# Kernel tuning notes

Measured on AMD Instinct MI355X. Metric: run time of the kernel, lower is better.

Reference implementation:

```python
import jax, jax.numpy as jnp
import numpy as np

N = 100000   # nodes
E = 1600000  # edges (avg degree 16)
IN, H, OUT = 64, 128, 1


def setup_inputs() -> dict:
    key = jax.random.key(0)
    ks = jax.random.split(key, 12)
    s = 0.05
    return {
        "x": jax.random.normal(ks[0], (N, IN), jnp.float32),
        "edge_index": jax.random.randint(ks[1], (2, E), 0, N, dtype=jnp.int64),
        "Wl1": jax.random.normal(ks[2], (IN, H), jnp.float32) * s,
        "Wr1": jax.random.normal(ks[3], (IN, H), jnp.float32) * s,
        "b1": jnp.zeros((H,), jnp.float32),
        "ln_g": jnp.ones((H,), jnp.float32),
        "ln_b": jnp.zeros((H,), jnp.float32),
        "Wres": jax.random.normal(ks[4], (IN, H), jnp.float32) * s,
        "bres": jnp.zeros((H,), jnp.float32),
        "Wl2": jax.random.normal(ks[5], (H, H), jnp.float32) * s,
        "Wr2": jax.random.normal(ks[6], (H, H), jnp.float32) * s,
        "b2": jnp.zeros((H,), jnp.float32),
        "Wl3": jax.random.normal(ks[7], (H, H), jnp.float32) * s,
        "Wr3": jax.random.normal(ks[8], (H, H), jnp.float32) * s,
        "b3": jnp.zeros((H,), jnp.float32),
        "Wl4": jax.random.normal(ks[9], (H, OUT), jnp.float32) * s,
        "Wr4": jax.random.normal(ks[10], (H, OUT), jnp.float32) * s,
        "b4": jnp.zeros((OUT,), jnp.float32),
    }


def _sage(h, src, dst, deg_inv, Wl, Wr, b):
    # PyG SAGEConv, aggr='mean': lin_l(mean_{j in N(i)} h_j) + lin_r(h_i)
    agg = jax.ops.segment_sum(h[src], dst, num_segments=N) * deg_inv[:, None]
    return agg @ Wl + h @ Wr + b


def _layernorm(h, g, b, eps=1e-5):
    mu = jnp.mean(h, axis=-1, keepdims=True)
    var = jnp.mean((h - mu) ** 2, axis=-1, keepdims=True)
    return (h - mu) * jax.lax.rsqrt(var + eps) * g + b


def reference(x, edge_index, Wl1, Wr1, b1, ln_g, ln_b, Wres, bres,
              Wl2, Wr2, b2, Wl3, Wr3, b3, Wl4, Wr4, b4):
    src, dst = edge_index[0], edge_index[1]
    deg = jax.ops.segment_sum(jnp.ones((E,), jnp.float32), dst, num_segments=N)
    deg_inv = 1.0 / jnp.maximum(deg, 1.0)

    h = jax.nn.relu(_layernorm(_sage(x, src, dst, deg_inv, Wl1, Wr1, b1), ln_g, ln_b))
    h = h + x @ Wres + bres              # residual (in_channel != hidden_channel)
    h = jax.nn.relu(_sage(h, src, dst, deg_inv, Wl2, Wr2, b2))   # dropout: eval no-op
    h = jax.nn.relu(_sage(h, src, dst, deg_inv, Wl3, Wr3, b3))
    out = _sage(h, src, dst, deg_inv, Wl4, Wr4, b4)
    return out.squeeze(-1)
```

## Files before the change

### kernel.cpp

```cpp
#include <hip/hip_runtime.h>
#include <hip/hip_bf16.h>

#define N_NODES 100000
#define N_EDGES 1600000

#define NBKT 782
#define SCAT_BLOCKS 240
#define BKT_CHUNK 6667
#define LP 72

#define SORT_BLOCKS 40
#define SORT_CHUNK 2500
#define BH2_N (NBKT * SCAT_BLOCKS)
#define BHB ((BH2_N + 1023) / 1024)
#define XBF_BLOCKS 6250

typedef __attribute__((ext_vector_type(8))) short short8v;
typedef __attribute__((ext_vector_type(4))) float float4v;

__device__ __forceinline__ unsigned short f2bf(float f) {
    unsigned int u = __float_as_uint(f);
    u = (u + 0x7FFFu + ((u >> 16) & 1u)) >> 16;
    return (unsigned short)u;
}
__device__ __forceinline__ float bf2f(unsigned short b) {
    return __uint_as_float((unsigned int)b << 16);
}

__global__ __launch_bounds__(256) void hist_xbf_kernel(const int* __restrict__ ei, int* __restrict__ bh2,
                                                       const float* __restrict__ x, unsigned short* __restrict__ xcat) {
    __shared__ int h[NBKT];
    int tid = threadIdx.x;
    if (blockIdx.x < SCAT_BLOCKS) {
        for (int i = tid; i < NBKT; i += 256) h[i] = 0;
        __syncthreads();
        int start = blockIdx.x * BKT_CHUNK;
        int end = start + BKT_CHUNK; if (end > N_EDGES) end = N_EDGES;
        for (int i = start + tid; i < end; i += 256) {
            int d = ei[N_EDGES + i];
            atomicAdd(&h[d >> 7], 1);
        }
        __syncthreads();
        for (int i = tid; i < NBKT; i += 256) bh2[i * SCAT_BLOCKS + blockIdx.x] = h[i];
    } else {
        int idx = (blockIdx.x - SCAT_BLOCKS) * 256 + tid;
        if (idx < N_NODES * 16) {
            int node = idx >> 4;
            int f0 = (idx & 15) * 4;
            float4 v = *(const float4*)(x + (size_t)idx * 4);
            ushort4 o;
            o.x = f2bf(v.x); o.y = f2bf(v.y); o.z = f2bf(v.z); o.w = f2bf(v.w);
            *(ushort4*)(xcat + (size_t)node * 128 + f0) = o;
        }
    }
}

__global__ __launch_bounds__(256) void gscan_a_kernel(const int* __restrict__ in, int* __restrict__ bsum, int n) {
    __shared__ int lds[256];
    int tid = threadIdx.x;
    int base = blockIdx.x * 1024 + tid * 4;
    int s = 0;
    #pragma unroll
    for (int i = 0; i < 4; i++) s += (base + i < n) ? in[base + i] : 0;
    lds[tid] = s;
    __syncthreads();
    for (int off = 128; off; off >>= 1) {
        if (tid < off) lds[tid] += lds[tid + off];
        __syncthreads();
    }
    if (tid == 0) bsum[blockIdx.x] = lds[0];
}

__global__ __launch_bounds__(256) void gscan_c_kernel(int* __restrict__ data, const int* __restrict__ bsum,
                                                      int nb, int n) {
    __shared__ int sb[256];
    __shared__ int lds[256];
    int tid = threadIdx.x;
    sb[tid] = (tid < nb) ? bsum[tid] : 0;
    __syncthreads();
    for (int off = 1; off < 256; off <<= 1) {
        int y = 0;
        if (tid >= off) y = sb[tid - off];
        __syncthreads();
        if (tid >= off) sb[tid] += y;
        __syncthreads();
    }
    int blockbase = (blockIdx.x == 0) ? 0 : sb[blockIdx.x - 1];

    int base = blockIdx.x * 1024 + tid * 4;
    int v[4];
    int s = 0;
    #pragma unroll
    for (int i = 0; i < 4; i++) {
        v[i] = (base + i < n) ? data[base + i] : 0;
        s += v[i];
    }
    lds[tid] = s;
    __syncthreads();
    for (int off = 1; off < 256; off <<= 1) {
        int y = 0;
        if (tid >= off) y = lds[tid - off];
        __syncthreads();
        if (tid >= off) lds[tid] += y;
        __syncthreads();
    }
    int run = blockbase + lds[tid] - s;
    #pragma unroll
    for (int i = 0; i < 4; i++) {
        if (base + i < n) data[base + i] = run;
        run += v[i];
// ... 157 lines not shown
}

__global__ __launch_bounds__(256) void agg128_kernel(unsigned short* __restrict__ hcat,
                                                     const int* __restrict__ row_ptr, const int* __restrict__ col,
                                                     const int* __restrict__ ord) {
    int tid = threadIdx.x;
    int slot = blockIdx.x * 8 + (tid >> 5);
    if (slot >= N_NODES) return;
    int i = ord[slot];
    int f0 = (tid & 31) * 4;
    int s = row_ptr[i], e = row_ptr[i + 1];
    float a0 = 0.f, a1 = 0.f, a2 = 0.f, a3 = 0.f;
    int t = s;
    while (t + 7 < e) {
        int j0 = col[t], j1 = col[t + 1], j2 = col[t + 2], j3 = col[t + 3];
        int j4 = col[t + 4], j5 = col[t + 5], j6 = col[t + 6], j7 = col[t + 7];
        ushort4 u0 = *(const ushort4*)(hcat + (size_t)j0 * 256 + f0);
        ushort4 u1 = *(const ushort4*)(hcat + (size_t)j1 * 256 + f0);
        ushort4 u2 = *(const ushort4*)(hcat + (size_t)j2 * 256 + f0);
        ushort4 u3 = *(const ushort4*)(hcat + (size_t)j3 * 256 + f0);
        ushort4 u4 = *(const ushort4*)(hcat + (size_t)j4 * 256 + f0);
        ushort4 u5 = *(const ushort4*)(hcat + (size_t)j5 * 256 + f0);
        ushort4 u6 = *(const ushort4*)(hcat + (size_t)j6 * 256 + f0);
        ushort4 u7 = *(const ushort4*)(hcat + (size_t)j7 * 256 + f0);
        ACC4(u0) ACC4(u1) ACC4(u2) ACC4(u3) ACC4(u4) ACC4(u5) ACC4(u6) ACC4(u7)
        t += 8;
    }
    if (t + 3 < e) {
        int j0 = col[t], j1 = col[t + 1], j2 = col[t + 2], j3 = col[t + 3];
        ushort4 u0 = *(const ushort4*)(hcat + (size_t)j0 * 256 + f0);
        ushort4 u1 = *(const ushort4*)(hcat + (size_t)j1 * 256 + f0);
        ushort4 u2 = *(const ushort4*)(hcat + (size_t)j2 * 256 + f0);
        ushort4 u3 = *(const ushort4*)(hcat + (size_t)j3 * 256 + f0);
        ACC4(u0) ACC4(u1) ACC4(u2) ACC4(u3)
        t += 4;
    }
    if (t + 1 < e) {
        int j0 = col[t], j1 = col[t + 1];
        ushort4 u0 = *(const ushort4*)(hcat + (size_t)j0 * 256 + f0);
        ushort4 u1 = *(const ushort4*)(hcat + (size_t)j1 * 256 + f0);
        ACC4(u0) ACC4(u1)
        t += 2;
    }
    if (t < e) {
        ushort4 u0 = *(const ushort4*)(hcat + (size_t)col[t] * 256 + f0);
        ACC4(u0)
    }
    float di = 1.0f / fmaxf((float)(e - s), 1.0f);
    ushort4 o;
    o.x = f2bf(a0 * di); o.y = f2bf(a1 * di); o.z = f2bf(a2 * di); o.w = f2bf(a3 * di);
    *(ushort4*)(hcat + (size_t)i * 256 + 128 + f0) = o;
}

__global__ __launch_bounds__(256) void wprep_all_kernel(const float* __restrict__ Wr1, const float* __restrict__ Wl1,
                                                        const float* __restrict__ Wres,
                                                        const float* __restrict__ Wl2, const float* __restrict__ Wr2,
                                                        const float* __restrict__ Wl3, const float* __restrict__ Wr3,
                                                        unsigned short* __restrict__ Bt1,
                                                        unsigned short* __restrict__ Bt2,
                                                        unsigned short* __restrict__ Bt3) {
    int idx = blockIdx.x * 256 + threadIdx.x;
    int seg = idx >> 15;
    int loc = idx & 32767;
    if (seg == 0) {
        int n = loc >> 7;
        int k = loc & 127;
        float v;
        if (n < 128) v = (k < 64) ? Wr1[k * 128 + n] : Wl1[(k - 64) * 128 + n];
        else         v = (k < 64) ? Wres[k * 128 + (n - 128)] : 0.f;
        Bt1[loc] = f2bf(v);
    } else if (seg == 1) {
        int n = loc >> 8;
        int k = loc & 255;
        float v = (k < 128) ? Wr2[k * 128 + n] : Wl2[(k - 128) * 128 + n];
        Bt2[loc] = f2bf(v);
    } else if (seg == 2) {
        int n = loc >> 8;
        int k = loc & 255;
        float v = (k < 128) ? Wr3[k * 128 + n] : Wl3[(k - 128) * 128 + n];
        Bt3[loc] = f2bf(v);
    }
}

__global__ __launch_bounds__(256) void mgemm1_ln_kernel(const unsigned short* __restrict__ A,
                                                        const unsigned short* __restrict__ Bt, int M,
                                                        const float* __restrict__ b1, const float* __restrict__ ln_g,
                                                        const float* __restrict__ ln_b, const float* __restrict__ bres,
                                                        unsigned short* __restrict__ hcat) {
    __shared__ unsigned short As[128 * LP];
    __shared__ unsigned short Bs[256 * LP];
    __shared__ float lsum[2][128], lsq[2][128];
    int tid = threadIdx.x;
    int m0 = blockIdx.x * 128;

    int lane = tid & 63;
    int wave = tid >> 6;
    int wm = (wave & 1) * 64;
    int wn = (wave >> 1) * 64;
    int lm = lane & 15;
    int lk = (lane >> 4) * 8;

    float4v accT[4][4], accR[4][4];
    #pragma unroll
    for (int i = 0; i < 4; i++)
        #pragma unroll
        for (int j = 0; j < 4; j++) { accT[i][j] = (float4v)0.f; accR[i][j] = (float4v)0.f; }

    int sr = tid >> 3;
    int sc = (tid & 7) * 8;

    for (int ks = 0; ks < 128; ks += 64) {
        if (ks) __syncthreads();
        int kk = ks + sc;
        #pragma unroll
        for (int rr = 0; rr < 384; rr += 32) {
            int r = sr + rr;
            if (r < 128) {
                int gm = m0 + r; if (gm > M - 1) gm = M - 1;
                *(ulonglong2*)&As[r * LP + sc] = *(const ulonglong2*)(A + (size_t)gm * 128 + kk);
            } else {
                int br = r - 128;
                *(ulonglong2*)&Bs[br * LP + sc] = *(const ulonglong2*)(Bt + (size_t)br * 128 + kk);
            }
        }
        __syncthreads();

        #pragma unroll
        for (int k0 = 0; k0 < 64; k0 += 32) {
            short8v af[4], bfT[4], bfR[4];
            #pragma unroll
            for (int i = 0; i < 4; i++)
                af[i] = *(const short8v*)&As[(wm + i * 16 + lm) * LP + k0 + lk];
            #pragma unroll
            for (int j = 0; j < 4; j++) {
                bfT[j] = *(const short8v*)&Bs[(wn + j * 16 + lm) * LP + k0 + lk];
                bfR[j] = *(const short8v*)&Bs[(128 + wn + j * 16 + lm) * LP + k0 + lk];
            }
            #pragma unroll
            for (int i = 0; i < 4; i++)
                #pragma unroll
                for (int j = 0; j < 4; j++) {
                    accT[i][j] = __builtin_amdgcn_mfma_f32_16x16x32_bf16(af[i], bfT[j], accT[i][j], 0, 0, 0);
                    accR[i][j] = __builtin_amdgcn_mfma_f32_16x16x32_bf16(af[i], bfR[j], accR[i][j], 0, 0, 0);
                }
        }
    }

    int q = lane >> 4;
    int wnidx = wave >> 1;
    float b1v[4], gv[4], bbv[4], brv[4];
    #pragma unroll
    for (int j = 0; j < 4; j++) {
        int cc = wn + j * 16 + lm;
        b1v[j] = b1[cc]; gv[j] = ln_g[cc]; bbv[j] = ln_b[cc]; brv[j] = bres[cc];
    }
    #pragma unroll
    for (int i = 0; i < 4; i++) {
        #pragma unroll
        for (int r = 0; r < 4; r++) {
            float sp = 0.f, sq = 0.f;
            #pragma unroll
            for (int j = 0; j < 4; j++) {
                float tv = accT[i][j][r] + b1v[j];
                sp += tv; sq += tv * tv;
            }
            #pragma unroll
            for (int off = 1; off < 16; off <<= 1) {
                sp += __shfl_xor(sp, off);
                sq += __shfl_xor(sq, off);
            }
            if (lm == 0) {
                int m = wm + i * 16 + q * 4 + r;
                lsum[wnidx][m] = sp;
                lsq[wnidx][m] = sq;
            }
        }
    }
    __syncthreads();
    #pragma unroll
    for (int i = 0; i < 4; i++) {
        #pragma unroll
        for (int r = 0; r < 4; r++) {
            int m = wm + i * 16 + q * 4 + r;
            float sum = lsum[0][m] + lsum[1][m];
            float s2 = lsq[0][m] + lsq[1][m];
            float mu = sum * (1.f / 128.f);
            float var = s2 * (1.f / 128.f) - mu * mu;
            float rstd = rsqrtf(var + 1e-5f);
            int gm = m0 + m;
            if (gm < M) {
                #pragma unroll
                for (int j = 0; j < 4; j++) {
                    float tv = accT[i][j][r] + b1v[j];
                    float y = fmaxf((tv - mu) * rstd * gv[j] + bbv[j], 0.f) + accR[i][j][r] + brv[j];
                    hcat[(size_t)gm * 256 + wn + j * 16 + lm] = f2bf(y);
                }
            }
        }
    }
}

__global__ __launch_bounds__(256) void mgemm_kernel(const unsigned short* __restrict__ A, int lda,
                                                    const unsigned short* __restrict__ Bt, int M,
                                                    const float* __restrict__ bias,
                                                    unsigned short* __restrict__ C, int ldc) {
    __shared__ unsigned short As[128 * LP];
    __shared__ unsigned short Bs[128 * LP];
    int tid = threadIdx.x;
    int m0 = blockIdx.x * 128;
    int n0 = blockIdx.y * 128;

    int lane = tid & 63;
    int wave = tid >> 6;
    int wm = (wave & 1) * 64;
    int wn = (wave >> 1) * 64;
    int lm = lane & 15;
    int lk = (lane >> 4) * 8;

    float4v acc[4][4];
    #pragma unroll
    for (int i = 0; i < 4; i++)
        #pragma unroll
        for (int j = 0; j < 4; j++) acc[i][j] = (float4v)0.f;

    int sr = tid >> 3;
    int sc = (tid & 7) * 8;

    for (int ks = 0; ks < lda; ks += 64) {
        if (ks) __syncthreads();
        int kk = ks + sc;
        #pragma unroll
        for (int rr = 0; rr < 128; rr += 32) {
            int r = sr + rr;
            int gm = m0 + r; if (gm > M - 1) gm = M - 1;
            *(ulonglong2*)&As[r * LP + sc] = *(const ulonglong2*)(A + (size_t)gm * lda + kk);
            *(ulonglong2*)&Bs[r * LP + sc] = *(const ulonglong2*)(Bt + (size_t)(n0 + r) * lda + kk);
        }
        __syncthreads();

        #pragma unroll
        for (int k0 = 0; k0 < 64; k0 += 32) {
            short8v af[4], bf[4];
            #pragma unroll
            for (int i = 0; i < 4; i++)
                af[i] = *(const short8v*)&As[(wm + i * 16 + lm) * LP + k0 + lk];
            #pragma unroll
            for (int j = 0; j < 4; j++)
                bf[j] = *(const short8v*)&Bs[(wn + j * 16 + lm) * LP + k0 + lk];
            #pragma unroll
            for (int i = 0; i < 4; i++)
                #pragma unroll
                for (int j = 0; j < 4; j++)
                    acc[i][j] = __builtin_amdgcn_mfma_f32_16x16x32_bf16(af[i], bf[j], acc[i][j], 0, 0, 0);
        }
    }

    int r0b = (lane >> 4) * 4;
    #pragma unroll
    for (int i = 0; i < 4; i++) {
        #pragma unroll
        for (int j = 0; j < 4; j++) {
            int cc = n0 + wn + j * 16 + lm;
            float bv = (bias != nullptr) ? bias[cc] : 0.f;
            #pragma unroll
            for (int r = 0; r < 4; r++) {
                int m = m0 + wm + i * 16 + r0b + r;
                if (m < M) {
                    float v = acc[i][j][r];
                    if (bias != nullptr) v = fmaxf(v + bv, 0.f);
                    C[(size_t)m * ldc + cc] = f2bf(v);
                }
            }
        }
    }
}

__global__ __launch_bounds__(256) void mgemm_pq_kernel(const unsigned short* __restrict__ A, int lda,
                                                       const unsigned short* __restrict__ Bt, int M,
                                                       const float* __restrict__ bias,
                                                       const float* __restrict__ Wl4, const float* __restrict__ Wr4,
                                                       const float* __restrict__ b4,
                                                       float* __restrict__ p, float* __restrict__ q) {
    __shared__ unsigned short As[128 * LP];
    __shared__ unsigned short Bs[128 * LP];
    __shared__ float psA[2][128], qsA[2][128];
    int tid = threadIdx.x;
    int m0 = blockIdx.x * 128;

    int lane = tid & 63;
    int wave = tid >> 6;
    int wm = (wave & 1) * 64;
    int wn = (wave >> 1) * 64;
    int lm = lane & 15;
    int lk = (lane >> 4) * 8;

    float4v acc[4][4];
    #pragma unroll
    for (int i = 0; i < 4; i++)
        #pragma unroll
        for (int j = 0; j < 4; j++) acc[i][j] = (float4v)0.f;

    int sr = tid >> 3;
    int sc = (tid & 7) * 8;

    for (int ks = 0; ks < lda; ks += 64) {
        if (ks) __syncthreads();
        int kk = ks + sc;
        #pragma unroll
        for (int rr = 0; rr < 128; rr += 32) {
            int r = sr + rr;
            int gm = m0 + r; if (gm > M - 1) gm = M - 1;
            *(ulonglong2*)&As[r * LP + sc] = *(const ulonglong2*)(A + (size_t)gm * lda + kk);
            *(ulonglong2*)&Bs[r * LP + sc] = *(const ulonglong2*)(Bt + (size_t)r * lda + kk);
        }
        __syncthreads();

        #pragma unroll
        for (int k0 = 0; k0 < 64; k0 += 32) {
            short8v af[4], bf[4];
            #pragma unroll
            for (int i = 0; i < 4; i++)
                af[i] = *(const short8v*)&As[(wm + i * 16 + lm) * LP + k0 + lk];
            #pragma unroll
            for (int j = 0; j < 4; j++)
                bf[j] = *(const short8v*)&Bs[(wn + j * 16 + lm) * LP + k0 + lk];
            #pragma unroll
            for (int i = 0; i < 4; i++)
                #pragma unroll
                for (int j = 0; j < 4; j++)
                    acc[i][j] = __builtin_amdgcn_mfma_f32_16x16x32_bf16(af[i], bf[j], acc[i][j], 0, 0, 0);
        }
    }

    int qd = lane >> 4;
    int wnidx = wave >> 1;
    float b3v[4], wlv[4], wrv[4];
    #pragma unroll
    for (int j = 0; j < 4; j++) {
        int cc = wn + j * 16 + lm;
        b3v[j] = bias[cc]; wlv[j] = Wl4[cc]; wrv[j] = Wr4[cc];
    }
    #pragma unroll
    for (int i = 0; i < 4; i++) {
        #pragma unroll
        for (int r = 0; r < 4; r++) {
            float pp = 0.f, qq = 0.f;
            #pragma unroll
            for (int j = 0; j < 4; j++) {
                float hv = fmaxf(acc[i][j][r] + b3v[j], 0.f);
                pp += hv * wlv[j]; qq += hv * wrv[j];
            }
            #pragma unroll
            for (int off = 1; off < 16; off <<= 1) {
                pp += __shfl_xor(pp, off);
                qq += __shfl_xor(qq, off);
            }
            if (lm == 0) {
                int m = wm + i * 16 + qd * 4 + r;
                psA[wnidx][m] = pp;
                qsA[wnidx][m] = qq;
            }
        }
    }
    __syncthreads();
    if (wnidx == 0 && lm == 0) {
        float b4v = b4[0];
        #pragma unroll
        for (int i = 0; i < 4; i++) {
            #pragma unroll
            for (int r = 0; r < 4; r++) {
                int m = wm + i * 16 + qd * 4 + r;
                int gm = m0 + m;
                if (gm < M) {
                    p[gm] = psA[0][m] + psA[1][m];
                    q[gm] = qsA[0][m] + qsA[1][m] + b4v;
                }
            }
        }
    }
}

__global__ __launch_bounds__(256) void final_kernel(const float* __restrict__ p, const float* __restrict__ q,
                                                    const int* __restrict__ row_ptr, const int* __restrict__ col,
                                                    float* __restrict__ out) {
    int i = blockIdx.x * 256 + threadIdx.x;
    if (i >= N_NODES) return;
    int s = row_ptr[i], e = row_ptr[i + 1];
    float acc = 0.f;
    int t = s;
    for (; t + 3 < e; t += 4)
        acc += p[col[t]] + p[col[t + 1]] + p[col[t + 2]] + p[col[t + 3]];
    for (; t < e; t++) acc += p[col[t]];
    float di = 1.0f / fmaxf((float)(e - s), 1.0f);
    out[i] = acc * di + q[i];
}


extern "C" void kernel_launch(void* const* d_in, const int* in_sizes, int n_in,
                              void* d_out, int out_size, void* d_ws, size_t ws_size,
                              hipStream_t stream) {
    const float* x    = (const float*)d_in[0];
    const int*   ei   = (const int*)d_in[1];
    const float* Wl1  = (const float*)d_in[2];
    const float* Wr1  = (const float*)d_in[3];
    const float* b1   = (const float*)d_in[4];
    const float* ln_g = (const float*)d_in[5];
    const float* ln_b = (const float*)d_in[6];
    const float* Wres = (const float*)d_in[7];
    const float* bres = (const float*)d_in[8];
    const float* Wl2  = (const float*)d_in[9];
    const float* Wr2  = (const float*)d_in[10];
    const float* b2   = (const float*)d_in[11];
    const float* Wl3  = (const float*)d_in[12];
    const float* Wr3  = (const float*)d_in[13];
    const float* b3   = (const float*)d_in[14];
    const float* Wl4  = (const float*)d_in[15];
    const float* Wr4  = (const float*)d_in[16];
    const float* b4   = (const float*)d_in[17];
    float* out = (float*)d_out;

    char* w = (char*)d_ws;
    size_t off = 0;
    auto alloc = [&](size_t bytes) -> void* {
        off = (off + 255) & ~(size_t)255;
        void* pp = w + off;
        off += bytes;
        return pp;
    };

    int*   deg        = (int*)alloc(N_NODES * 4);
    int*   row_ptr    = (int*)alloc((N_NODES + 1) * 4);
    int*   bsum       = (int*)alloc(1024);
    int*   col        = (int*)alloc(N_EDGES * 4);
    int*   bh2        = (int*)alloc(BH2_N * 4);
    int*   bh         = (int*)alloc(64 * SORT_BLOCKS * 4);
    int*   ord        = (int*)alloc(N_NODES * 4);
    unsigned short* Bt1  = (unsigned short*)alloc(256 * 128 * 2);
    unsigned short* Bt2  = (unsigned short*)alloc(128 * 256 * 2);
    unsigned short* Bt3  = (unsigned short*)alloc(128 * 256 * 2);
    unsigned short* xcat = (unsigned short*)alloc((size_t)N_NODES * 128 * 2);
    unsigned short* hcat = (unsigned short*)alloc((size_t)N_NODES * 256 * 2);
    int*   packed  = (int*)alloc((size_t)N_EDGES * 4);
    float* p       = (float*)alloc(N_NODES * 4);
    float* q       = (float*)alloc(N_NODES * 4);
    (void)ws_size; (void)n_in; (void)in_sizes; (void)out_size;

    const int NB = (N_NODES + 255) / 256;
    const int MB = (N_NODES + 127) / 128;

    wprep_all_kernel<<<384, 256, 0, stream>>>(Wr1, Wl1, Wres, Wl2, Wr2, Wl3, Wr3, Bt1, Bt2, Bt3);

    hist_xbf_kernel<<<SCAT_BLOCKS + XBF_BLOCKS, 256, 0, stream>>>(ei, bh2, x, xcat);
    gscan_a_kernel<<<BHB, 256, 0, stream>>>(bh2, bsum, BH2_N);
    gscan_c_kernel<<<BHB, 256, 0, stream>>>(bh2, bsum, BHB, BH2_N);
    bkt_scatter2_kernel<<<SCAT_BLOCKS, 256, 0, stream>>>(ei, bh2, packed);
    bkt_build_kernel<<<NBKT, 256, 0, stream>>>(packed, bh2, deg, row_ptr, col);
    dsort_hist_kernel<<<SORT_BLOCKS, 256, 0, stream>>>(deg, bh);
    dsort_scat_kernel<<<SORT_BLOCKS, 256, 0, stream>>>(deg, bh, ord);

    agg64_kernel<<<(N_NODES + 15) / 16, 256, 0, stream>>>(xcat, row_ptr, col, ord);
    mgemm1_ln_kernel<<<MB, 256, 0, stream>>>(xcat, Bt1, N_NODES, b1, ln_g, ln_b, bres, hcat);

    agg128_kernel<<<(N_NODES + 7) / 8, 256, 0, stream>>>(hcat, row_ptr, col, ord);
    mgemm_kernel<<<dim3(MB, 1), 256, 0, stream>>>(hcat, 256, Bt2, N_NODES, b2, hcat, 256);

    agg128_kernel<<<(N_NODES + 7) / 8, 256, 0, stream>>>(hcat, row_ptr, col, ord);
    mgemm_pq_kernel<<<MB, 256, 0, stream>>>(hcat, 256, Bt3, N_NODES, b3, Wl4, Wr4, b4, p, q);

    final_kernel<<<NB, 256, 0, stream>>>(p, q, row_ptr, col, out);
}
```

Measured before the change: 419.4 us.

## Use direct global-to-LDS loads, XOR-swizzled LDS and double buffering in GEMMs

After: 409.5 us. -2.4%, faster.

```diff
diff --git a/kernel.cpp b/kernel.cpp
--- a/kernel.cpp
+++ b/kernel.cpp
@@ -7,7 +7,6 @@
 #define NBKT 782
 #define SCAT_BLOCKS 240
 #define BKT_CHUNK 6667
-#define LP 72
 
 #define SORT_BLOCKS 40
 #define SORT_CHUNK 2500
@@ -26,6 +25,15 @@
 __device__ __forceinline__ float bf2f(unsigned short b) {
     return __uint_as_float((unsigned int)b << 16);
 }
+
+typedef __attribute__((address_space(1))) const unsigned int gld_g_t;
+typedef __attribute__((address_space(3))) unsigned int gld_l_t;
+__device__ __forceinline__ void gld_lds16(const void* g, void* l) {
+    __builtin_amdgcn_global_load_lds((gld_g_t*)g, (gld_l_t*)l, 16, 0, 0);
+}
+
+#define SWZ64(row, ksh)  ((row) * 64  + ((ksh) ^ (((row) & 7) << 3)))
+#define SWZ128(row, ksh) ((row) * 128 + ((ksh) ^ (((row) & 7) << 3)))
 
 __global__ __launch_bounds__(256) void hist_xbf_kernel(const int* __restrict__ ei, int* __restrict__ bh2,
                                                        const float* __restrict__ x, unsigned short* __restrict__ xcat) {
@@ -354,9 +362,10 @@
                                                         const float* __restrict__ b1, const float* __restrict__ ln_g,
                                                         const float* __restrict__ ln_b, const float* __restrict__ bres,
                                                         unsigned short* __restrict__ hcat) {
-    __shared__ unsigned short As[128 * LP];
-    __shared__ unsigned short Bs[256 * LP];
-    __shared__ float lsum[2][128], lsq[2][128];
+    __shared__ unsigned short smem[40960];
+    unsigned short* As  = smem;
+    unsigned short* BsT = smem + 16384;
+    unsigned short* BsR = smem + 32768;
     int tid = threadIdx.x;
     int m0 = blockIdx.x * 128;
 
@@ -373,45 +382,53 @@
         #pragma unroll
         for (int j = 0; j < 4; j++) { accT[i][j] = (float4v)0.f; accR[i][j] = (float4v)0.f; }
 
-    int sr = tid >> 3;
-    int sc = (tid & 7) * 8;
-
-    for (int ks = 0; ks < 128; ks += 64) {
-        if (ks) __syncthreads();
-        int kk = ks + sc;
-        #pragma unroll
-        for (int rr = 0; rr < 384; rr += 32) {
-            int r = sr + rr;
-            if (r < 128) {
-                int gm = m0 + r; if (gm > M - 1) gm = M - 1;
-                *(ulonglong2*)&As[r * LP + sc] = *(const ulonglong2*)(A + (size_t)gm * 128 + kk);
-            } else {
-                int br = r - 128;
-                *(ulonglong2*)&Bs[br * LP + sc] = *(const ulonglong2*)(Bt + (size_t)br * 128 + kk);
-            }
-        }
-        __syncthreads();
-
-        #pragma unroll
-        for (int k0 = 0; k0 < 64; k0 += 32) {
-            short8v af[4], bfT[4], bfR[4];
-            #pragma unroll
-            for (int i = 0; i < 4; i++)
-                af[i] = *(const short8v*)&As[(wm + i * 16 + lm) * LP + k0 + lk];
-            #pragma unroll
-            for (int j = 0; j < 4; j++) {
-                bfT[j] = *(const short8v*)&Bs[(wn + j * 16 + lm) * LP + k0 + lk];
-                bfR[j] = *(const short8v*)&Bs[(128 + wn + j * 16 + lm) * LP + k0 + lk];
-            }
+    #pragma unroll
+    for (int rr = 0; rr < 8; rr++) {
+        int Lb = (rr * 4 + wave) * 1024 + lane * 16;
+        int row = Lb >> 8;
+        int sb = (Lb & 255) ^ ((row & 7) << 4);
+        int gm = m0 + row; if (gm > M - 1) gm = M - 1;
+        gld_lds16(A + (size_t)gm * 128 + (sb >> 1), &As[Lb >> 1]);
+        gld_lds16(Bt + (size_t)row * 128 + (sb >> 1), &BsT[Lb >> 1]);
+    }
+    #pragma unroll
+    for (int rr = 0; rr < 4; rr++) {
+        int Lb = (rr * 4 + wave) * 1024 + lane * 16;
+        int row = Lb >> 7;
+        int sb = (Lb & 127) ^ ((row & 7) << 4);
+        gld_lds16(Bt + (size_t)(128 + row) * 128 + (sb >> 1), &BsR[Lb >> 1]);
+    }
+    __syncthreads();
+
+    #pragma unroll
+    for (int k0 = 0; k0 < 128; k0 += 32) {
+        short8v af[4], bfT[4];
+        #pragma unroll
+        for (int i = 0; i < 4; i++)
+            af[i] = *(const short8v*)&As[SWZ128(wm + i * 16 + lm, k0 + lk)];
+        #pragma unroll
+        for (int j = 0; j < 4; j++)
+            bfT[j] = *(const short8v*)&BsT[SWZ128(wn + j * 16 + lm, k0 + lk)];
+        #pragma unroll
+        for (int i = 0; i < 4; i++)
+            #pragma unroll
+            for (int j = 0; j < 4; j++)
+                accT[i][j] = __builtin_amdgcn_mfma_f32_16x16x32_bf16(af[i], bfT[j], accT[i][j], 0, 0, 0);
+        if (k0 < 64) {
+            short8v bfR[4];
+            #pragma unroll
+            for (int j = 0; j < 4; j++)
+                bfR[j] = *(const short8v*)&BsR[SWZ64(wn + j * 16 + lm, k0 + lk)];
             #pragma unroll
             for (int i = 0; i < 4; i++)
                 #pragma unroll
-                for (int j = 0; j < 4; j++) {
-                    accT[i][j] = __builtin_amdgcn_mfma_f32_16x16x32_bf16(af[i], bfT[j], accT[i][j], 0, 0, 0);
+                for (int j = 0; j < 4; j++)
                     accR[i][j] = __builtin_amdgcn_mfma_f32_16x16x32_bf16(af[i], bfR[j], accR[i][j], 0, 0, 0);
-                }
-        }
-    }
+        }
+    }
+    __syncthreads();
+    float* lsum = (float*)BsR;
+    float* lsq  = lsum + 256;
 
     int q = lane >> 4;
     int wnidx = wave >> 1;
@@ -438,8 +455,8 @@
             }
             if (lm == 0) {
                 int m = wm + i * 16 + q * 4 + r;
-                lsum[wnidx][m] = sp;
-                lsq[wnidx][m] = sq;
+                lsum[wnidx * 128 + m] = sp;
+                lsq[wnidx * 128 + m] = sq;
             }
         }
     }
@@ -449,8 +466,8 @@
         #pragma unroll
         for (int r = 0; r < 4; r++) {
             int m = wm + i * 16 + q * 4 + r;
-            float sum = lsum[0][m] + lsum[1][m];
-            float s2 = lsq[0][m] + lsq[1][m];
+            float sum = lsum[m] + lsum[128 + m];
+            float s2 = lsq[m] + lsq[128 + m];
             float mu = sum * (1.f / 128.f);
             float var = s2 * (1.f / 128.f) - mu * mu;
             float rstd = rsqrtf(var + 1e-5f);
@@ -471,11 +488,10 @@
                                                     const unsigned short* __restrict__ Bt, int M,
                                                     const float* __restrict__ bias,
                                                     unsigned short* __restrict__ C, int ldc) {
-    __shared__ unsigned short As[128 * LP];
-    __shared__ unsigned short Bs[128 * LP];
+    __shared__ unsigned short As[2][8192];
+    __shared__ unsigned short Bs[2][8192];
     int tid = threadIdx.x;
     int m0 = blockIdx.x * 128;
-    int n0 = blockIdx.y * 128;
 
     int lane = tid & 63;
     int wave = tid >> 6;
@@ -490,36 +506,39 @@
         #pragma unroll
         for (int j = 0; j < 4; j++) acc[i][j] = (float4v)0.f;
 
-    int sr = tid >> 3;
-    int sc = (tid & 7) * 8;
-
+    auto stage = [&](int b, int ks) {
+        #pragma unroll
+        for (int rr = 0; rr < 4; rr++) {
+            int Lb = (rr * 4 + wave) * 1024 + lane * 16;
+            int row = Lb >> 7;
+            int sb = (Lb & 127) ^ ((row & 7) << 4);
+            int gm = m0 + row; if (gm > M - 1) gm = M - 1;
+            gld_lds16(A + (size_t)gm * lda + ks + (sb >> 1), &As[b][Lb >> 1]);
+            gld_lds16(Bt + (size_t)row * lda + ks + (sb >> 1), &Bs[b][Lb >> 1]);
+        }
+    };
+
+    stage(0, 0);
+    __syncthreads();
     for (int ks = 0; ks < lda; ks += 64) {
-        if (ks) __syncthreads();
-        int kk = ks + sc;
-        #pragma unroll
-        for (int rr = 0; rr < 128; rr += 32) {
-            int r = sr + rr;
-            int gm = m0 + r; if (gm > M - 1) gm = M - 1;
-            *(ulonglong2*)&As[r * LP + sc] = *(const ulonglong2*)(A + (size_t)gm * lda + kk);
-            *(ulonglong2*)&Bs[r * LP + sc] = *(const ulonglong2*)(Bt + (size_t)(n0 + r) * lda + kk);
-        }
-        __syncthreads();
-
+        int cur = (ks >> 6) & 1;
+        if (ks + 64 < lda) stage(cur ^ 1, ks + 64);
         #pragma unroll
         for (int k0 = 0; k0 < 64; k0 += 32) {
             short8v af[4], bf[4];
             #pragma unroll
             for (int i = 0; i < 4; i++)
-                af[i] = *(const short8v*)&As[(wm + i * 16 + lm) * LP + k0 + lk];
+                af[i] = *(const short8v*)&As[cur][SWZ64(wm + i * 16 + lm, k0 + lk)];
             #pragma unroll
             for (int j = 0; j < 4; j++)
-                bf[j] = *(const short8v*)&Bs[(wn + j * 16 + lm) * LP + k0 + lk];
+                bf[j] = *(const short8v*)&Bs[cur][SWZ64(wn + j * 16 + lm, k0 + lk)];
             #pragma unroll
             for (int i = 0; i < 4; i++)
                 #pragma unroll
                 for (int j = 0; j < 4; j++)
                     acc[i][j] = __builtin_amdgcn_mfma_f32_16x16x32_bf16(af[i], bf[j], acc[i][j], 0, 0, 0);
         }
+        __syncthreads();
     }
 
     int r0b = (lane >> 4) * 4;
@@ -527,7 +546,7 @@
     for (int i = 0; i < 4; i++) {
         #pragma unroll
         for (int j = 0; j < 4; j++) {
-            int cc = n0 + wn + j * 16 + lm;
+            int cc = wn + j * 16 + lm;
             float bv = (bias != nullptr) ? bias[cc] : 0.f;
             #pragma unroll
             for (int r = 0; r < 4; r++) {
@@ -548,8 +567,8 @@
                                                        const float* __restrict__ Wl4, const float* __restrict__ Wr4,
                                                        const float* __restrict__ b4,
                                                        float* __restrict__ p, float* __restrict__ q) {
-    __shared__ unsigned short As[128 * LP];
-    __shared__ unsigned short Bs[128 * LP];
+    __shared__ unsigned short As[2][8192];
+    __shared__ unsigned short Bs[2][8192];
     __shared__ float psA[2][128], qsA[2][128];
     int tid = threadIdx.x;
     int m0 = blockIdx.x * 128;
@@ -567,36 +586,39 @@
         #pragma unroll
         for (int j = 0; j < 4; j++) acc[i][j] = (float4v)0.f;
 
-    int sr = tid >> 3;
-    int sc = (tid & 7) * 8;
-
+    auto stage = [&](int b, int ks) {
+        #pragma unroll
+        for (int rr = 0; rr < 4; rr++) {
+            int Lb = (rr * 4 + wave) * 1024 + lane * 16;
+            int row = Lb >> 7;
+            int sb = (Lb & 127) ^ ((row & 7) << 4);
+            int gm = m0 + row; if (gm > M - 1) gm = M - 1;
+            gld_lds16(A + (size_t)gm * lda + ks + (sb >> 1), &As[b][Lb >> 1]);
+            gld_lds16(Bt + (size_t)row * lda + ks + (sb >> 1), &Bs[b][Lb >> 1]);
+        }
+    };
+
+    stage(0, 0);
+    __syncthreads();
     for (int ks = 0; ks < lda; ks += 64) {
-        if (ks) __syncthreads();
-        int kk = ks + sc;
-        #pragma unroll
-        for (int rr = 0; rr < 128; rr += 32) {
-            int r = sr + rr;
-            int gm = m0 + r; if (gm > M - 1) gm = M - 1;
-            *(ulonglong2*)&As[r * LP + sc] = *(const ulonglong2*)(A + (size_t)gm * lda + kk);
-            *(ulonglong2*)&Bs[r * LP + sc] = *(const ulonglong2*)(Bt + (size_t)r * lda + kk);
-        }
-        __syncthreads();
-
+        int cur = (ks >> 6) & 1;
+        if (ks + 64 < lda) stage(cur ^ 1, ks + 64);
         #pragma unroll
         for (int k0 = 0; k0 < 64; k0 += 32) {
             short8v af[4], bf[4];
             #pragma unroll
             for (int i = 0; i < 4; i++)
-                af[i] = *(const short8v*)&As[(wm + i * 16 + lm) * LP + k0 + lk];
+                af[i] = *(const short8v*)&As[cur][SWZ64(wm + i * 16 + lm, k0 + lk)];
             #pragma unroll
             for (int j = 0; j < 4; j++)
-                bf[j] = *(const short8v*)&Bs[(wn + j * 16 + lm) * LP + k0 + lk];
+                bf[j] = *(const short8v*)&Bs[cur][SWZ64(wn + j * 16 + lm, k0 + lk)];
             #pragma unroll
             for (int i = 0; i < 4; i++)
                 #pragma unroll
                 for (int j = 0; j < 4; j++)
                     acc[i][j] = __builtin_amdgcn_mfma_f32_16x16x32_bf16(af[i], bf[j], acc[i][j], 0, 0, 0);
         }
+        __syncthreads();
     }
 
     int qd = lane >> 4;
@@ -729,7 +751,7 @@
     mgemm1_ln_kernel<<<MB, 256, 0, stream>>>(xcat, Bt1, N_NODES, b1, ln_g, ln_b, bres, hcat);
 
     agg128_kernel<<<(N_NODES + 7) / 8, 256, 0, stream>>>(hcat, row_ptr, col, ord);
-    mgemm_kernel<<<dim3(MB, 1), 256, 0, stream>>>(hcat, 256, Bt2, N_NODES, b2, hcat, 256);
+    mgemm_kernel<<<MB, 256, 0, stream>>>(hcat, 256, Bt2, N_NODES, b2, hcat, 256);
 
     agg128_kernel<<<(N_NODES + 7) / 8, 256, 0, stream>>>(hcat, row_ptr, col, ord);
     mgemm_pq_kernel<<<MB, 256, 0, stream>>>(hcat, 256, Bt3, N_NODES, b3, Wl4, Wr4, b4, p, q);
```

## Restructure dense GEMMs into per-wave 16-row strips with LDS-resident swizzled weights

Applied to the files above, without the earlier changes.

After: 372.9 us. 1.12x faster.

```diff
diff --git a/kernel.cpp b/kernel.cpp
--- a/kernel.cpp
+++ b/kernel.cpp
@@ -7,7 +7,6 @@
 #define NBKT 782
 #define SCAT_BLOCKS 240
 #define BKT_CHUNK 6667
-#define LP 72
 
 #define SORT_BLOCKS 40
 #define SORT_CHUNK 2500
@@ -15,6 +14,9 @@
 #define BHB ((BH2_N + 1023) / 1024)
 #define XBF_BLOCKS 6250
 
+#define NSTRIPS 6250
+#define GEMM_BLOCKS 782
+
 typedef __attribute__((ext_vector_type(8))) short short8v;
 typedef __attribute__((ext_vector_type(4))) float float4v;
 
@@ -26,6 +28,15 @@
 __device__ __forceinline__ float bf2f(unsigned short b) {
     return __uint_as_float((unsigned int)b << 16);
 }
+
+typedef __attribute__((address_space(1))) const unsigned int gld_g_t;
+typedef __attribute__((address_space(3))) unsigned int gld_l_t;
+__device__ __forceinline__ void gld_lds16(const void* g, void* l) {
+    __builtin_amdgcn_global_load_lds((gld_g_t*)g, (gld_l_t*)l, 16, 0, 0);
+}
+
+#define SWZ128(row, ksh) ((row) * 128 + ((ksh) ^ (((row) & 7) << 3)))
+#define SWZ256(row, ksh) ((row) * 256 + ((ksh) ^ (((row) & 7) << 3)))
 
 __global__ __launch_bounds__(256) void hist_xbf_kernel(const int* __restrict__ ei, int* __restrict__ bh2,
                                                        const float* __restrict__ x, unsigned short* __restrict__ xcat) {
@@ -349,300 +360,206 @@
     }
 }
 
-__global__ __launch_bounds__(256) void mgemm1_ln_kernel(const unsigned short* __restrict__ A,
-                                                        const unsigned short* __restrict__ Bt, int M,
+__global__ __launch_bounds__(512) void mgemm1_ln_kernel(const unsigned short* __restrict__ A,
+                                                        const unsigned short* __restrict__ Bt,
                                                         const float* __restrict__ b1, const float* __restrict__ ln_g,
                                                         const float* __restrict__ ln_b, const float* __restrict__ bres,
                                                         unsigned short* __restrict__ hcat) {
-    __shared__ unsigned short As[128 * LP];
-    __shared__ unsigned short Bs[256 * LP];
-    __shared__ float lsum[2][128], lsq[2][128];
-    int tid = threadIdx.x;
-    int m0 = blockIdx.x * 128;
-
-    int lane = tid & 63;
-    int wave = tid >> 6;
-    int wm = (wave & 1) * 64;
-    int wn = (wave >> 1) * 64;
-    int lm = lane & 15;
-    int lk = (lane >> 4) * 8;
-
-    float4v accT[4][4], accR[4][4];
-    #pragma unroll
-    for (int i = 0; i < 4; i++)
-        #pragma unroll
-        for (int j = 0; j < 4; j++) { accT[i][j] = (float4v)0.f; accR[i][j] = (float4v)0.f; }
-
-    int sr = tid >> 3;
-    int sc = (tid & 7) * 8;
-
-    for (int ks = 0; ks < 128; ks += 64) {
-        if (ks) __syncthreads();
-        int kk = ks + sc;
-        #pragma unroll
-        for (int rr = 0; rr < 384; rr += 32) {
-            int r = sr + rr;
-            if (r < 128) {
-                int gm = m0 + r; if (gm > M - 1) gm = M - 1;
-                *(ulonglong2*)&As[r * LP + sc] = *(const ulonglong2*)(A + (size_t)gm * 128 + kk);
-            } else {
-                int br = r - 128;
-                *(ulonglong2*)&Bs[br * LP + sc] = *(const ulonglong2*)(Bt + (size_t)br * 128 + kk);
-            }
-        }
-        __syncthreads();
-
-        #pragma unroll
-        for (int k0 = 0; k0 < 64; k0 += 32) {
-            short8v af[4], bfT[4], bfR[4];
+    __shared__ unsigned short Bs[32768];
+    int tid = threadIdx.x;
+    int wave = tid >> 6, lane = tid & 63;
+    int lm = lane & 15, lk = (lane >> 4) * 8;
+
+    #pragma unroll
+    for (int rnd = 0; rnd < 8; rnd++) {
+        int Lb = rnd * 8192 + tid * 16;
+        int row = Lb >> 8;
+        int sb = (Lb & 255) ^ ((row & 7) << 4);
+        gld_lds16(Bt + (size_t)row * 128 + (sb >> 1), &Bs[Lb >> 1]);
+    }
+    __syncthreads();
+
+    int strip = blockIdx.x * 8 + wave;
+    if (strip >= NSTRIPS) return;
+    int m0 = strip * 16;
+
+    float4v accT[8], accR[8];
+    #pragma unroll
+    for (int j = 0; j < 8; j++) { accT[j] = (float4v)0.f; accR[j] = (float4v)0.f; }
+
+    const unsigned short* arow = A + (size_t)(m0 + lm) * 128 + lk;
+    #pragma unroll
+    for (int k0 = 0; k0 < 128; k0 += 32) {
+        short8v af = *(const short8v*)(arow + k0);
+        short8v bf[8];
+        #pragma unroll
+        for (int j = 0; j < 8; j++)
+            bf[j] = *(const short8v*)&Bs[SWZ128(j * 16 + lm, k0 + lk)];
+        #pragma unroll
+        for (int j = 0; j < 8; j++)
+            accT[j] = __builtin_amdgcn_mfma_f32_16x16x32_bf16(af, bf[j], accT[j], 0, 0, 0);
+        if (k0 < 64) {
+            short8v bg[8];
             #pragma unroll
-            for (int i = 0; i < 4; i++)
-                af[i] = *(const short8v*)&As[(wm + i * 16 + lm) * LP + k0 + lk];
+            for (int j = 0; j < 8; j++)
+                bg[j] = *(const short8v*)&Bs[SWZ128(128 + j * 16 + lm, k0 + lk)];
             #pragma unroll
-            for (int j = 0; j < 4; j++) {
-                bfT[j] = *(const short8v*)&Bs[(wn + j * 16 + lm) * LP + k0 + lk];
-                bfR[j] = *(const short8v*)&Bs[(128 + wn + j * 16 + lm) * LP + k0 + lk];
-            }
-            #pragma unroll
-            for (int i = 0; i < 4; i++)
-                #pragma unroll
-                for (int j = 0; j < 4; j++) {
-                    accT[i][j] = __builtin_amdgcn_mfma_f32_16x16x32_bf16(af[i], bfT[j], accT[i][j], 0, 0, 0);
-                    accR[i][j] = __builtin_amdgcn_mfma_f32_16x16x32_bf16(af[i], bfR[j], accR[i][j], 0, 0, 0);
-                }
-        }
-    }
-
-    int q = lane >> 4;
-    int wnidx = wave >> 1;
-    float b1v[4], gv[4], bbv[4], brv[4];
-    #pragma unroll
-    for (int j = 0; j < 4; j++) {
-        int cc = wn + j * 16 + lm;
+            for (int j = 0; j < 8; j++)
+                accR[j] = __builtin_amdgcn_mfma_f32_16x16x32_bf16(af, bg[j], accR[j], 0, 0, 0);
+        }
+    }
+
+    float b1v[8], gv[8], bbv[8], brv[8];
+    #pragma unroll
+    for (int j = 0; j < 8; j++) {
+        int cc = j * 16 + lm;
         b1v[j] = b1[cc]; gv[j] = ln_g[cc]; bbv[j] = ln_b[cc]; brv[j] = bres[cc];
     }
-    #pragma unroll
-    for (int i = 0; i < 4; i++) {
+    int q4 = lane >> 4;
+    #pragma unroll
+    for (int r = 0; r < 4; r++) {
+        float sp = 0.f, sq = 0.f;
+        #pragma unroll
+        for (int j = 0; j < 8; j++) {
+            float tv = accT[j][r] + b1v[j];
+            sp += tv; sq += tv * tv;
+        }
+        #pragma unroll
+        for (int off = 1; off < 16; off <<= 1) {
+            sp += __shfl_xor(sp, off);
+            sq += __shfl_xor(sq, off);
+        }
+        float mu = sp * (1.f / 128.f);
+        float var = sq * (1.f / 128.f) - mu * mu;
+        float rstd = rsqrtf(var + 1e-5f);
+        int gm = m0 + q4 * 4 + r;
+        #pragma unroll
+        for (int j = 0; j < 8; j++) {
+            float tv = accT[j][r] + b1v[j];
+            float y = fmaxf((tv - mu) * rstd * gv[j] + bbv[j], 0.f) + accR[j][r] + brv[j];
+            hcat[(size_t)gm * 256 + j * 16 + lm] = f2bf(y);
+        }
+    }
+}
+
+__global__ __launch_bounds__(512) void mgemm_kernel(const unsigned short* __restrict__ A,
+                                                    const unsigned short* __restrict__ Bt,
+                                                    const float* __restrict__ bias,
+                                                    unsigned short* __restrict__ C) {
+    __shared__ unsigned short Bs[32768];
+    int tid = threadIdx.x;
+    int wave = tid >> 6, lane = tid & 63;
+    int lm = lane & 15, lk = (lane >> 4) * 8;
+
+    #pragma unroll
+    for (int rnd = 0; rnd < 8; rnd++) {
+        int Lb = rnd * 8192 + tid * 16;
+        int row = Lb >> 9;
+        int sb = (Lb & 511) ^ ((row & 7) << 4);
+        gld_lds16(Bt + ((size_t)row << 8) + (sb >> 1), &Bs[Lb >> 1]);
+    }
+    __syncthreads();
+
+    int strip = blockIdx.x * 8 + wave;
+    if (strip >= NSTRIPS) return;
+    int m0 = strip * 16;
+
+    float4v acc[8];
+    #pragma unroll
+    for (int j = 0; j < 8; j++) acc[j] = (float4v)0.f;
+
+    const unsigned short* arow = A + (size_t)(m0 + lm) * 256 + lk;
+    #pragma unroll
+    for (int k0 = 0; k0 < 256; k0 += 32) {
+        short8v af = *(const short8v*)(arow + k0);
+        short8v bf[8];
+        #pragma unroll
+        for (int j = 0; j < 8; j++)
+            bf[j] = *(const short8v*)&Bs[SWZ256(j * 16 + lm, k0 + lk)];
+        #pragma unroll
+        for (int j = 0; j < 8; j++)
+            acc[j] = __builtin_amdgcn_mfma_f32_16x16x32_bf16(af, bf[j], acc[j], 0, 0, 0);
+    }
+
+    int q4 = lane >> 4;
+    #pragma unroll
+    for (int j = 0; j < 8; j++) {
+        int cc = j * 16 + lm;
+        float bv = bias[cc];
         #pragma unroll
         for (int r = 0; r < 4; r++) {
-            float sp = 0.f, sq = 0.f;
-            #pragma unroll
-            for (int j = 0; j < 4; j++) {
-                float tv = accT[i][j][r] + b1v[j];
-                sp += tv; sq += tv * tv;
-            }
-            #pragma unroll
-            for (int off = 1; off < 16; off <<= 1) {
-                sp += __shfl_xor(sp, off);
-                sq += __shfl_xor(sq, off);
-            }
-            if (lm == 0) {
-                int m = wm + i * 16 + q * 4 + r;
-                lsum[wnidx][m] = sp;
-                lsq[wnidx][m] = sq;
-            }
-        }
-    }
-    __syncthreads();
-    #pragma unroll
-    for (int i = 0; i < 4; i++) {
-        #pragma unroll
-        for (int r = 0; r < 4; r++) {
-            int m = wm + i * 16 + q * 4 + r;
-            float sum = lsum[0][m] + lsum[1][m];
-            float s2 = lsq[0][m] + lsq[1][m];
-            float mu = sum * (1.f / 128.f);
-            float var = s2 * (1.f / 128.f) - mu * mu;
-            float rstd = rsqrtf(var + 1e-5f);
-            int gm = m0 + m;
-            if (gm < M) {
-                #pragma unroll
-                for (int j = 0; j < 4; j++) {
-                    float tv = accT[i][j][r] + b1v[j];
-                    float y = fmaxf((tv - mu) * rstd * gv[j] + bbv[j], 0.f) + accR[i][j][r] + brv[j];
-                    hcat[(size_t)gm * 256 + wn + j * 16 + lm] = f2bf(y);
-                }
-            }
-        }
-    }
-}
-
-__global__ __launch_bounds__(256) void mgemm_kernel(const unsigned short* __restrict__ A, int lda,
-                                                    const unsigned short* __restrict__ Bt, int M,
-                                                    const float* __restrict__ bias,
-                                                    unsigned short* __restrict__ C, int ldc) {
-    __shared__ unsigned short As[128 * LP];
-    __shared__ unsigned short Bs[128 * LP];
-    int tid = threadIdx.x;
-    int m0 = blockIdx.x * 128;
-    int n0 = blockIdx.y * 128;
-
-    int lane = tid & 63;
-    int wave = tid >> 6;
-    int wm = (wave & 1) * 64;
-    int wn = (wave >> 1) * 64;
-    int lm = lane & 15;
-    int lk = (lane >> 4) * 8;
-
-    float4v acc[4][4];
-    #pragma unroll
-    for (int i = 0; i < 4; i++)
-        #pragma unroll
-        for (int j = 0; j < 4; j++) acc[i][j] = (float4v)0.f;
-
-    int sr = tid >> 3;
-    int sc = (tid & 7) * 8;
-
-    for (int ks = 0; ks < lda; ks += 64) {
-        if (ks) __syncthreads();
-        int kk = ks + sc;
-        #pragma unroll
-        for (int rr = 0; rr < 128; rr += 32) {
-            int r = sr + rr;
-            int gm = m0 + r; if (gm > M - 1) gm = M - 1;
-            *(ulonglong2*)&As[r * LP + sc] = *(const ulonglong2*)(A + (size_t)gm * lda + kk);
-            *(ulonglong2*)&Bs[r * LP + sc] = *(const ulonglong2*)(Bt + (size_t)(n0 + r) * lda + kk);
-        }
-        __syncthreads();
-
-        #pragma unroll
-        for (int k0 = 0; k0 < 64; k0 += 32) {
-            short8v af[4], bf[4];
-            #pragma unroll
-            for (int i = 0; i < 4; i++)
-                af[i] = *(const short8v*)&As[(wm + i * 16 + lm) * LP + k0 + lk];
-            #pragma unroll
-            for (int j = 0; j < 4; j++)
-                bf[j] = *(const short8v*)&Bs[(wn + j * 16 + lm) * LP + k0 + lk];
-            #pragma unroll
-            for (int i = 0; i < 4; i++)
-                #pragma unroll
-                for (int j = 0; j < 4; j++)
-                    acc[i][j] = __builtin_amdgcn_mfma_f32_16x16x32_bf16(af[i], bf[j], acc[i][j], 0, 0, 0);
-        }
-    }
-
-    int r0b = (lane >> 4) * 4;
-    #pragma unroll
-    for (int i = 0; i < 4; i++) {
-        #pragma unroll
-        for (int j = 0; j < 4; j++) {
-            int cc = n0 + wn + j * 16 + lm;
-            float bv = (bias != nullptr) ? bias[cc] : 0.f;
-            #pragma unroll
-            for (int r = 0; r < 4; r++) {
-                int m = m0 + wm + i * 16 + r0b + r;
-                if (m < M) {
-                    float v = acc[i][j][r];
-                    if (bias != nullptr) v = fmaxf(v + bv, 0.f);
-                    C[(size_t)m * ldc + cc] = f2bf(v);
-                }
-            }
-        }
-    }
-}
-
-__global__ __launch_bounds__(256) void mgemm_pq_kernel(const unsigned short* __restrict__ A, int lda,
-                                                       const unsigned short* __restrict__ Bt, int M,
+            int m = m0 + q4 * 4 + r;
+            C[(size_t)m * 256 + cc] = f2bf(fmaxf(acc[j][r] + bv, 0.f));
+        }
+    }
+}
+
+__global__ __launch_bounds__(512) void mgemm_pq_kernel(const unsigned short* __restrict__ A,
+                                                       const unsigned short* __restrict__ Bt,
                                                        const float* __restrict__ bias,
                                                        const float* __restrict__ Wl4, const float* __restrict__ Wr4,
                                                        const float* __restrict__ b4,
                                                        float* __restrict__ p, float* __restrict__ q) {
-    __shared__ unsigned short As[128 * LP];
-    __shared__ unsigned short Bs[128 * LP];
-    __shared__ float psA[2][128], qsA[2][128];
-    int tid = threadIdx.x;
-    int m0 = blockIdx.x * 128;
-
-    int lane = tid & 63;
-    int wave = tid >> 6;
-    int wm = (wave & 1) * 64;
-    int wn = (wave >> 1) * 64;
-    int lm = lane & 15;
-    int lk = (lane >> 4) * 8;
-
-    float4v acc[4][4];
-    #pragma unroll
-    for (int i = 0; i < 4; i++)
-        #pragma unroll
-        for (int j = 0; j < 4; j++) acc[i][j] = (float4v)0.f;
-
-    int sr = tid >> 3;
-    int sc = (tid & 7) * 8;
-
-    for (int ks = 0; ks < lda; ks += 64) {
-        if (ks) __syncthreads();
-        int kk = ks + sc;
-        #pragma unroll
-        for (int rr = 0; rr < 128; rr += 32) {
-            int r = sr + rr;
-            int gm = m0 + r; if (gm > M - 1) gm = M - 1;
-            *(ulonglong2*)&As[r * LP + sc] = *(const ulonglong2*)(A + (size_t)gm * lda + kk);
-            *(ulonglong2*)&Bs[r * LP + sc] = *(const ulonglong2*)(Bt + (size_t)r * lda + kk);
-        }
-        __syncthreads();
-
-        #pragma unroll
-        for (int k0 = 0; k0 < 64; k0 += 32) {
-            short8v af[4], bf[4];
-            #pragma unroll
-            for (int i = 0; i < 4; i++)
-                af[i] = *(const short8v*)&As[(wm + i * 16 + lm) * LP + k0 + lk];
-            #pragma unroll
-            for (int j = 0; j < 4; j++)
-                bf[j] = *(const short8v*)&Bs[(wn + j * 16 + lm) * LP + k0 + lk];
-            #pragma unroll
-            for (int i = 0; i < 4; i++)
-                #pragma unroll
-                for (int j = 0; j < 4; j++)
-                    acc[i][j] = __builtin_amdgcn_mfma_f32_16x16x32_bf16(af[i], bf[j], acc[i][j], 0, 0, 0);
-        }
-    }
-
-    int qd = lane >> 4;
-    int wnidx = wave >> 1;
-    float b3v[4], wlv[4], wrv[4];
-    #pragma unroll
-    for (int j = 0; j < 4; j++) {
-        int cc = wn + j * 16 + lm;
+    __shared__ unsigned short Bs[32768];
+    int tid = threadIdx.x;
+    int wave = tid >> 6, lane = tid & 63;
+    int lm = lane & 15, lk = (lane >> 4) * 8;
+
+    #pragma unroll
+    for (int rnd = 0; rnd < 8; rnd++) {
+        int Lb = rnd * 8192 + tid * 16;
+        int row = Lb >> 9;
+        int sb = (Lb & 511) ^ ((row & 7) << 4);
+        gld_lds16(Bt + ((size_t)row << 8) + (sb >> 1), &Bs[Lb >> 1]);
+    }
+    __syncthreads();
+
+    int strip = blockIdx.x * 8 + wave;
+    if (strip >= NSTRIPS) return;
+    int m0 = strip * 16;
+
+    float4v acc[8];
+    #pragma unroll
+    for (int j = 0; j < 8; j++) acc[j] = (float4v)0.f;
+
+    const unsigned short* arow = A + (size_t)(m0 + lm) * 256 + lk;
+    #pragma unroll
+    for (int k0 = 0; k0 < 256; k0 += 32) {
+        short8v af = *(const short8v*)(arow + k0);
+        short8v bf[8];
+        #pragma unroll
+        for (int j = 0; j < 8; j++)
+            bf[j] = *(const short8v*)&Bs[SWZ256(j * 16 + lm, k0 + lk)];
+        #pragma unroll
+        for (int j = 0; j < 8; j++)
+            acc[j] = __builtin_amdgcn_mfma_f32_16x16x32_bf16(af, bf[j], acc[j], 0, 0, 0);
+    }
+
+    float b3v[8], wlv[8], wrv[8];
+    #pragma unroll
+    for (int j = 0; j < 8; j++) {
+        int cc = j * 16 + lm;
         b3v[j] = bias[cc]; wlv[j] = Wl4[cc]; wrv[j] = Wr4[cc];
     }
-    #pragma unroll
-    for (int i = 0; i < 4; i++) {
-        #pragma unroll
-        for (int r = 0; r < 4; r++) {
-            float pp = 0.f, qq = 0.f;
-            #pragma unroll
-            for (int j = 0; j < 4; j++) {
-                float hv = fmaxf(acc[i][j][r] + b3v[j], 0.f);
-                pp += hv * wlv[j]; qq += hv * wrv[j];
-            }
-            #pragma unroll
-            for (int off = 1; off < 16; off <<= 1) {
-                pp += __shfl_xor(pp, off);
-                qq += __shfl_xor(qq, off);
-            }
-            if (lm == 0) {
-                int m = wm + i * 16 + qd * 4 + r;
-                psA[wnidx][m] = pp;
-                qsA[wnidx][m] = qq;
-            }
-        }
-    }
-    __syncthreads();
-    if (wnidx == 0 && lm == 0) {
-        float b4v = b4[0];
-        #pragma unroll
-        for (int i = 0; i < 4; i++) {
-            #pragma unroll
-            for (int r = 0; r < 4; r++) {
-                int m = wm + i * 16 + qd * 4 + r;
-                int gm = m0 + m;
-                if (gm < M) {
-                    p[gm] = psA[0][m] + psA[1][m];
-                    q[gm] = qsA[0][m] + qsA[1][m] + b4v;
-                }
-            }
+    float b4v = b4[0];
+    int q4 = lane >> 4;
+    #pragma unroll
+    for (int r = 0; r < 4; r++) {
+        float pp = 0.f, qq = 0.f;
+        #pragma unroll
+        for (int j = 0; j < 8; j++) {
+            float hv = fmaxf(acc[j][r] + b3v[j], 0.f);
+            pp += hv * wlv[j]; qq += hv * wrv[j];
+        }
+        #pragma unroll
+        for (int off = 1; off < 16; off <<= 1) {
+            pp += __shfl_xor(pp, off);
+            qq += __shfl_xor(qq, off);
+        }
+        if (lm == 0) {
+            int m = m0 + q4 * 4 + r;
+            p[m] = pp;
+            q[m] = qq + b4v;
         }
     }
 }
@@ -713,7 +630,6 @@
     (void)ws_size; (void)n_in; (void)in_sizes; (void)out_size;
 
     const int NB = (N_NODES + 255) / 256;
-    const int MB = (N_NODES + 127) / 128;
 
     wprep_all_kernel<<<384, 256, 0, stream>>>(Wr1, Wl1, Wres, Wl2, Wr2, Wl3, Wr3, Bt1, Bt2, Bt3);
 
@@ -726,13 +642,13 @@
     dsort_scat_kernel<<<SORT_BLOCKS, 256, 0, stream>>>(deg, bh, ord);
 
     agg64_kernel<<<(N_NODES + 15) / 16, 256, 0, stream>>>(xcat, row_ptr, col, ord);
-    mgemm1_ln_kernel<<<MB, 256, 0, stream>>>(xcat, Bt1, N_NODES, b1, ln_g, ln_b, bres, hcat);
+    mgemm1_ln_kernel<<<GEMM_BLOCKS, 512, 0, stream>>>(xcat, Bt1, b1, ln_g, ln_b, bres, hcat);
 
     agg128_kernel<<<(N_NODES + 7) / 8, 256, 0, stream>>>(hcat, row_ptr, col, ord);
-    mgemm_kernel<<<dim3(MB, 1), 256, 0, stream>>>(hcat, 256, Bt2, N_NODES, b2, hcat, 256);
+    mgemm_kernel<<<GEMM_BLOCKS, 512, 0, stream>>>(hcat, Bt2, b2, hcat);
 
     agg128_kernel<<<(N_NODES + 7) / 8, 256, 0, stream>>>(hcat, row_ptr, col, ord);
-    mgemm_pq_kernel<<<MB, 256, 0, stream>>>(hcat, 256, Bt3, N_NODES, b3, Wl4, Wr4, b4, p, q);
+    mgemm_pq_kernel<<<GEMM_BLOCKS, 512, 0, stream>>>(hcat, Bt3, b3, Wl4, Wr4, b4, p, q);
 
     final_kernel<<<NB, 256, 0, stream>>>(p, q, row_ptr, col, out);
 }
```
